# Performance work log

Measured on AMD Instinct MI355X. Metric: run time of the kernel, lower is better.

Reference implementation:

```python
import jax, jax.numpy as jnp
import numpy as np

N, E = 100000, 1600000          # nodes, edges
H, DH = 8, 256                  # heads, dim_hidden
D = DH // H                     # dim per head
NEG_SLOPE = 0.2                 # GAT leaky_relu slope
BETA = 0.5


def setup_inputs() -> dict:
    key = jax.random.key(0)
    ks = jax.random.split(key, 10)
    s = 1.0 / np.sqrt(DH)
    return {
        "x": jax.random.normal(ks[0], (N, DH), jnp.float32),
        "edge_index": jax.random.randint(ks[1], (2, E), 0, N, jnp.int32),
        "edge_attr": jax.random.uniform(ks[2], (E,), jnp.float32),
        # GAT params (no bias, add_self_loops=False)
        "Wg": jax.random.normal(ks[3], (DH, DH), jnp.float32) * s,
        "att_src": jax.random.normal(ks[4], (H, D), jnp.float32) * s,
        "att_dst": jax.random.normal(ks[5], (H, D), jnp.float32) * s,
        # h_lin
        "Wh": jax.random.normal(ks[6], (DH, DH), jnp.float32) * s,
        "bh": jnp.zeros((DH,), jnp.float32),
        # lin
        "Wl": jax.random.normal(ks[7], (DH, DH), jnp.float32) * s,
        "bl": jnp.zeros((DH,), jnp.float32),
        # LayerNorm
        "ln_g": jnp.ones((DH,), jnp.float32),
        "ln_b": jnp.zeros((DH,), jnp.float32),
        # beta gate (beta>=0 -> constant vector)
        "b_param": jnp.full((DH,), BETA, jnp.float32),
    }


def _layer_norm(v, g, b, eps=1e-5):
    mu = jnp.mean(v, axis=-1, keepdims=True)
    var = jnp.var(v, axis=-1, keepdims=True)
    return (v - mu) * jax.lax.rsqrt(var + eps) * g + b


def _weighted_gat(x, edge_index, edge_attr, Wg, att_src, att_dst):
    # GATConv with per-edge weights folded into the softmax numerator.
    xs = (x @ Wg).reshape(N, H, D)                       # [N,H,D]
    a_src = jnp.einsum("nhd,hd->nh", xs, att_src)        # [N,H]
    a_dst = jnp.einsum("nhd,hd->nh", xs, att_dst)
    src, dst = edge_index[0], edge_index[1]
    e = jax.nn.leaky_relu(a_src[src] + a_dst[dst], NEG_SLOPE)   # [E,H]
    m = jax.ops.segment_max(e, dst, num_segments=N)             # [N,H]
    m = jnp.where(jnp.isfinite(m), m, 0.0)                      # isolated nodes
    p = jnp.exp(e - m[dst]) * edge_attr[:, None]                # weighted exp
    denom = jax.ops.segment_sum(p, dst, num_segments=N)         # [N,H]
    alpha = p / (denom[dst] + 1e-16)                            # [E,H]
    msg = alpha[:, :, None] * xs[src]                           # [E,H,D]
    out = jax.ops.segment_sum(msg, dst, num_segments=N)         # [N,H,D]
    return out.reshape(N, DH)


def reference(x, edge_index, edge_attr, Wg, att_src, att_dst, Wh, bh, Wl, bl, ln_g, ln_b, b_param):
    x_in = x
    h = jax.nn.relu(x @ Wh + bh)
    xg = _weighted_gat(x, edge_index, edge_attr, Wg, att_src, att_dst) + (x @ Wl + bl)
    xg = jax.nn.relu(xg)                                  # dropout p=0 (eval)
    beta = b_param[None, :]
    out = (1.0 - beta) * _layer_norm(h * xg, ln_g, ln_b) + beta * xg
    return out + x_in                                     # residual=True
```

## Files before the change

### kernel.cpp

```cpp
#include <hip/hip_runtime.h>

typedef __attribute__((ext_vector_type(4))) float f32x4;
typedef __attribute__((ext_vector_type(8))) __bf16 bf16x8;

__device__ __forceinline__ unsigned short f2bf(float f) {
    return __builtin_bit_cast(unsigned short, (__bf16)f);
}
__device__ __forceinline__ float bf2f(unsigned short u) {
    return __builtin_bit_cast(float, (unsigned)u << 16);
}

__device__ __forceinline__ void gload16(const void* g, void* l) {
    __builtin_amdgcn_global_load_lds(
        (const __attribute__((address_space(1))) void*)g,
        (__attribute__((address_space(3))) void*)l, 16, 0, 0);
}

__global__ __launch_bounds__(256) void k_prep(
    const float* __restrict__ x, unsigned short* __restrict__ xb, long total, long totalPad,
    const float* __restrict__ Wg, const float* __restrict__ Wh, const float* __restrict__ Wl,
    unsigned short* __restrict__ wt,
    const int* __restrict__ dst, int E, int* __restrict__ deg,
    int nCvt, int nHist) {
    const int b = blockIdx.x;
    const int tid = threadIdx.x;
    if (b < nCvt) {
        long i = ((long)b * 256 + tid) * 4;
        if (i >= totalPad) return;
        if (i < total) {
            float4 v = *(const float4*)(x + i);
            ushort4 u;
            u.x = f2bf(v.x); u.y = f2bf(v.y); u.z = f2bf(v.z); u.w = f2bf(v.w);
            *(ushort4*)(xb + i) = u;
        } else {
            ushort4 u = {0, 0, 0, 0};
            *(ushort4*)(xb + i) = u;
        }
    } else if (b < nCvt + 768) {
        int t = (b - nCvt) * 256 + tid;
        int nn = t >> 8, k = t & 255;
        const float* W = (nn < 256) ? Wg : (nn < 512) ? Wh : Wl;
        wt[t] = f2bf(W[k * 256 + (nn & 255)]);
    } else {
        int bb = b - nCvt - 768;
        for (int e = bb * 256 + tid; e < E; e += nHist * 256)
            atomicAdd(&deg[dst[e]], 1);
    }
}

__global__ __launch_bounds__(256) void k_gemm(
    const unsigned short* __restrict__ A,
    const unsigned short* __restrict__ BT,
    unsigned short* __restrict__ xs, unsigned short* __restrict__ hb,
    unsigned short* __restrict__ xlb,
    const float* __restrict__ bh, const float* __restrict__ bl, int M, int nwg) {
    __shared__ unsigned short Al[128 * 32];
    __shared__ unsigned short Bl[128 * 32];
    const int bid = blockIdx.x;
    const int xcd = bid & 7, idx = bid >> 3;
    const int q = nwg >> 3, r = nwg & 7;
    const int wg = (xcd < r ? xcd * (q + 1) : r * (q + 1) + (xcd - r) * q) + idx;
    const int tm = wg / 6, tn = wg % 6;

    const int tid = threadIdx.x;
    const int lane = tid & 63;
    const int wave = tid >> 6;
    const int wm = (wave >> 1) * 64, wn = (wave & 1) * 64;

    f32x4 acc[4][4] = {};

    const int ml = tid & 15;
    const int kh = (tid >> 4) & 3;
    const int m0 = (tid >> 6) * 16 + ml;
    const unsigned short* Ag = A + (size_t)tm * 128 * 256 + (size_t)m0 * 256 + kh * 8;
    const unsigned short* Bg = BT + (size_t)tn * 128 * 256 + (size_t)m0 * 256 + kh * 8;

    const char* Ab = (const char*)Al + (wm >> 4) * 1024 + lane * 16;
    const char* Bb = (const char*)Bl + (wn >> 4) * 1024 + lane * 16;

    for (int ks = 0; ks < 8; ++ks) {
        const int k0 = ks * 32;
#pragma unroll
        for (int s = 0; s < 2; ++s) {
            gload16(Ag + (size_t)s * 64 * 256 + k0, (char*)Al + s * 4096 + wave * 1024 + (lane * 16));
            gload16(Bg + (size_t)s * 64 * 256 + k0, (char*)Bl + s * 4096 + wave * 1024 + (lane * 16));
        }
        __syncthreads();
        bf16x8 af[4], bfr[4];
#pragma unroll
        for (int i = 0; i < 4; ++i) {
            af[i]  = *(const bf16x8*)(Ab + i * 1024);
            bfr[i] = *(const bf16x8*)(Bb + i * 1024);
        }
#pragma unroll
        for (int i = 0; i < 4; ++i)
#pragma unroll
            for (int j = 0; j < 4; ++j)
                acc[i][j] = __builtin_amdgcn_mfma_f32_16x16x32_bf16(af[i], bfr[j], acc[i][j], 0, 0, 0);
        __syncthreads();
    }

    const int colbase = tn * 128 + wn;
    const int rbase = tm * 128 + wm + (lane >> 4) * 4;
#pragma unroll
    for (int i = 0; i < 4; ++i) {
#pragma unroll
        for (int j = 0; j < 4; ++j) {
            const int cg = colbase + j * 16 + (lane & 15);
#pragma unroll
            for (int q2 = 0; q2 < 4; ++q2) {
                const int rg = rbase + i * 16 + q2;
                if (rg < M) {
                    float v = acc[i][j][q2];
                    if (cg < 256) {
                        xs[(size_t)rg * 256 + cg] = f2bf(v);
                    } else if (cg < 512) {
                        float t = v + bh[cg - 256];
                        hb[(size_t)rg * 256 + (cg - 256)] = f2bf(t > 0.f ? t : 0.f);
                    } else {
                        xlb[(size_t)rg * 256 + (cg - 512)] = f2bf(v + bl[cg - 512]);
                    }
                }
            }
        }
    }
}

__global__ __launch_bounds__(256) void k_attn(const unsigned short* __restrict__ xs,
                                              const float* __restrict__ att_src,
                                              const float* __restrict__ att_dst,
                                              float* __restrict__ a_src,
                                              float* __restrict__ a_dst, int N) {
    int t = blockIdx.x * 256 + threadIdx.x;
    int n = t >> 3, hh = t & 7;
    if (n >= N) return;
    const ushort4* xp = (const ushort4*)(xs + (size_t)n * 256 + hh * 32);
    const float4* sp = (const float4*)(att_src + hh * 32);
    const float4* dp = (const float4*)(att_dst + hh * 32);
    float sa = 0.f, sd = 0.f;
#pragma unroll
    for (int q = 0; q < 8; ++q) {
        ushort4 u = xp[q];
        float4 s = sp[q], d = dp[q];
        float v0 = bf2f(u.x), v1 = bf2f(u.y), v2 = bf2f(u.z), v3 = bf2f(u.w);
        sa += v0 * s.x + v1 * s.y + v2 * s.z + v3 * s.w;
        sd += v0 * d.x + v1 * d.y + v2 * d.z + v3 * d.w;
    }
    a_src[t] = sa;
    a_dst[t] = sd;
}

__global__ __launch_bounds__(256) void k_scan1(const int* __restrict__ deg, int* __restrict__ offs,
                                               int* __restrict__ bsum, int Npad) {
    __shared__ int s[256];
    int t = threadIdx.x;
    int i = blockIdx.x * 256 + t;
    int v = (i < Npad) ? ((deg[i] + 7) & ~7) : 0;
    s[t] = v;
    __syncthreads();
#pragma unroll
    for (int off = 1; off < 256; off <<= 1) {
        int x = (t >= off) ? s[t - off] : 0;
        __syncthreads();
        s[t] += x;
        __syncthreads();
    }
    offs[i] = s[t] - v;
    if (t == 255) bsum[blockIdx.x] = s[255];
}

__global__ __launch_bounds__(512) void k_scan2(int* __restrict__ bsum, int nb) {
    __shared__ int s[512];
    int t = threadIdx.x;
    int v = (t < nb) ? bsum[t] : 0;
    s[t] = v;
    __syncthreads();
#pragma unroll
    for (int off = 1; off < 512; off <<= 1) {
        int x = (t >= off) ? s[t - off] : 0;
        __syncthreads();
        s[t] += x;
        __syncthreads();
    }
    if (t < nb) bsum[t] = s[t] - v;
}

__global__ __launch_bounds__(256) void k_scan3(int* __restrict__ offs, const int* __restrict__ bsum,
                                               int* __restrict__ cursor) {
    int i = blockIdx.x * 256 + threadIdx.x;
    int o = offs[i] + bsum[blockIdx.x];
    offs[i] = o;
    cursor[i] = o;
}

__global__ void k_edge(const int* __restrict__ ei, const float* __restrict__ ea, int E,
                       const float* __restrict__ a_src, const float* __restrict__ a_dst,
                       int* __restrict__ cursor, int* __restrict__ srcArr,
                       unsigned short* __restrict__ pvArr) {
    for (int e = blockIdx.x * blockDim.x + threadIdx.x; e < E; e += gridDim.x * blockDim.x) {
        const int s = ei[e];
        const int d = ei[(size_t)E + e];
        const float w = ea[e];
        const int pos = atomicAdd(&cursor[d], 1);
        const float4* As = (const float4*)(a_src + (size_t)s * 8);
        const float4* Ad = (const float4*)(a_dst + (size_t)d * 8);
        float4 s0 = As[0], s1 = As[1], d0 = Ad[0], d1 = Ad[1];
        float a[8] = {s0.x + d0.x, s0.y + d0.y, s0.z + d0.z, s0.w + d0.w,
                      s1.x + d1.x, s1.y + d1.y, s1.z + d1.z, s1.w + d1.w};
        unsigned pk[4];
#pragma unroll
        for (int h = 0; h < 4; ++h) {
            float lo = a[2 * h], hi = a[2 * h + 1];
            lo = (lo > 0.f) ? lo : 0.2f * lo;
            hi = (hi > 0.f) ? hi : 0.2f * hi;
            unsigned short plo = f2bf(__expf(lo) * w);
            unsigned short phi = f2bf(__expf(hi) * w);
            pk[h] = (unsigned)plo | ((unsigned)phi << 16);
        }
        srcArr[pos] = s;
        uint4 v = {pk[0], pk[1], pk[2], pk[3]};
        *(uint4*)(pvArr + (size_t)pos * 8) = v;
    }
}

__global__ __launch_bounds__(256) void k_agg(
    const int* __restrict__ offs, const int* __restrict__ deg,
    const int* __restrict__ srcArr, const unsigned short* __restrict__ pvArr,
    const unsigned short* __restrict__ xs, const unsigned short* __restrict__ hb,
    const unsigned short* __restrict__ xlb,
    const unsigned short* __restrict__ xbf, const float* __restrict__ ln_g,
    const float* __restrict__ ln_b,
    const float* __restrict__ beta, float* __restrict__ out, int N) {
    const int wave = threadIdx.x >> 6, lane = threadIdx.x & 63;
    const int n = blockIdx.x * 4 + wave;
    if (n >= N) return;
    const int start = offs[n];
    const int dpad = (deg[n] + 7) & ~7;
    const int head = lane >> 3;
    const int eSub = lane & 7;

    f32x4 acc = {0.f, 0.f, 0.f, 0.f};
    float dsum = 0.f;

    const int* sp = srcArr + start;
    const unsigned short* pp = pvArr + (size_t)start * 8 + head;
    const char* xsb = (const char*)xs;
    const unsigned rowoff = (unsigned)lane * 8;

    for (int g = 0; g < dpad; g += 8) {
        const int sA = sp[g + eSub];
        ushort4 rows[8];
        float pvv[8];
#pragma unroll
        for (int e = 0; e < 8; ++e)
            rows[e] = *(const ushort4*)(xsb + (size_t)(unsigned)__shfl(sA, e) * 512 + rowoff);
#pragma unroll
        for (int e = 0; e < 8; ++e)
            pvv[e] = bf2f(pp[(size_t)(g + e) * 8]);
#pragma unroll
        for (int e = 0; e < 8; ++e) {
            const float p = pvv[e];
            dsum += p;
            acc[0] += p * bf2f(rows[e].x);
            acc[1] += p * bf2f(rows[e].y);
            acc[2] += p * bf2f(rows[e].z);
            acc[3] += p * bf2f(rows[e].w);
        }
    }
    const float inv = 1.f / (dsum + 1e-16f);

    const size_t base = (size_t)n * 256 + lane * 4;
    ushort4 xlu = *(const ushort4*)(xlb + base);
    ushort4 hu = *(const ushort4*)(hb + base);
    ushort4 xiu = *(const ushort4*)(xbf + base);
    f32x4 xg, t4;
    float s1 = 0.f, s2 = 0.f;
    const float xl0[4] = {bf2f(xlu.x), bf2f(xlu.y), bf2f(xlu.z), bf2f(xlu.w)};
    const float hv0[4] = {bf2f(hu.x), bf2f(hu.y), bf2f(hu.z), bf2f(hu.w)};
    const float xi0[4] = {bf2f(xiu.x), bf2f(xiu.y), bf2f(xiu.z), bf2f(xiu.w)};
#pragma unroll
    for (int q = 0; q < 4; ++q) {
        float gg = acc[q] * inv + xl0[q];
        gg = gg > 0.f ? gg : 0.f;
        xg[q] = gg;
        float t = hv0[q] * gg;
        t4[q] = t;
        s1 += t;
        s2 += t * t;
    }
#pragma unroll
    for (int off = 32; off; off >>= 1) {
        s1 += __shfl_xor(s1, off);
        s2 += __shfl_xor(s2, off);
    }
    const float mu = s1 * (1.f / 256.f);
    const float var = s2 * (1.f / 256.f) - mu * mu;
    const float rs = rsqrtf(var + 1e-5f);

    f32x4 g4 = *(const f32x4*)(ln_g + lane * 4);
    f32x4 b4 = *(const f32x4*)(ln_b + lane * 4);
    f32x4 be = *(const f32x4*)(beta + lane * 4);
    f32x4 o;
#pragma unroll
    for (int q = 0; q < 4; ++q) {
        float ln = (t4[q] - mu) * rs * g4[q] + b4[q];
        o[q] = (1.f - be[q]) * ln + be[q] * xg[q] + xi0[q];
    }
    *(f32x4*)(out + base) = o;
}

extern "C" void kernel_launch(void* const* d_in, const int* in_sizes, int n_in,
                              void* d_out, int out_size, void* d_ws, size_t ws_size,
                              hipStream_t stream) {
    const float* x = (const float*)d_in[0];
    const int* ei = (const int*)d_in[1];
    const float* ea = (const float*)d_in[2];
    const float* Wg = (const float*)d_in[3];
    const float* att_src = (const float*)d_in[4];
    const float* att_dst = (const float*)d_in[5];
    const float* Wh = (const float*)d_in[6];
    const float* bh = (const float*)d_in[7];
    const float* Wl = (const float*)d_in[8];
    const float* bl = (const float*)d_in[9];
    const float* ln_g = (const float*)d_in[10];
    const float* ln_b = (const float*)d_in[11];
    const float* beta = (const float*)d_in[12];
    float* out = (float*)d_out;

    const int DH = 256;
    const int N = in_sizes[0] / DH;
    const int E = in_sizes[2];
    const int Mpad = ((N + 127) / 128) * 128;
    const int Npad = ((N + 255) / 256) * 256;
    const int nscanb = Npad / 256;
    const int nwg = (Mpad / 128) * 6;
    const int nCvt = Mpad / 4;
    const int nHist = 2048;
    const size_t Epad = (size_t)E + 8 * (size_t)N;

    char* w = (char*)d_ws;
    auto take = [&](size_t bytes) -> char* {
        char* p = w;
        w += (bytes + 255) & ~(size_t)255;
        return p;
    };
    unsigned short* xs = (unsigned short*)take((size_t)N * DH * 2);
    unsigned short* hb = (unsigned short*)take((size_t)N * DH * 2);
    unsigned short* xlb = (unsigned short*)take((size_t)N * DH * 2);
    float* a_src = (float*)take((size_t)N * 8 * 4);
    float* a_dst = (float*)take((size_t)N * 8 * 4);
    unsigned short* xbf = (unsigned short*)take((size_t)Mpad * DH * 2);
    unsigned short* wt = (unsigned short*)take((size_t)768 * 256 * 2);
    int* deg = (int*)take((size_t)Npad * 4);
    int* offs = (int*)take((size_t)Npad * 4);
    int* cursor = (int*)take((size_t)Npad * 4);
    int* bsum = (int*)take(512 * 4);
    int* srcArr = (int*)take(Epad * 4);
    unsigned short* pvArr = (unsigned short*)take(Epad * 8 * 2);

    hipMemsetAsync(deg, 0, (size_t)Npad * 4, stream);
    hipMemsetAsync(srcArr, 0, Epad * 4, stream);
    hipMemsetAsync(pvArr, 0, Epad * 8 * 2, stream);

    k_prep<<<nCvt + 768 + nHist, 256, 0, stream>>>(x, xbf, (long)N * DH, (long)Mpad * DH,
                                                   Wg, Wh, Wl, wt, ei + E, E, deg, nCvt, nHist);

    k_scan1<<<nscanb, 256, 0, stream>>>(deg, offs, bsum, Npad);
    k_scan2<<<1, 512, 0, stream>>>(bsum, nscanb);
    k_scan3<<<nscanb, 256, 0, stream>>>(offs, bsum, cursor);

    k_gemm<<<nwg, 256, 0, stream>>>(xbf, wt, xs, hb, xlb, bh, bl, N, nwg);

    k_attn<<<(N * 8 + 255) / 256, 256, 0, stream>>>(xs, att_src, att_dst, a_src, a_dst, N);

    k_edge<<<2048, 256, 0, stream>>>(ei, ea, E, a_src, a_dst, cursor, srcArr, pvArr);

    k_agg<<<(N + 3) / 4, 256, 0, stream>>>(offs, deg, srcArr, pvArr,
                                           xs, hb, xlb, xbf, ln_g, ln_b, beta, out, N);
}
```

Measured before the change: 606.8 us.

## Restructure GEMM to 8 waves, double-buffer A in LDS, read B from global

The GEMM block grows to 512 threads, with each wave computing a 32x64 sub-tile. The A tile is double-buffered in LDS so the next k-slice loads while the current one computes, dropping one barrier per iteration. B fragments now come straight from global memory, relying on cache, instead of being staged through LDS. The epilogue picks the output buffer and bias once per block rather than branching per element. The risks are extra global and L2 traffic for B and higher register pressure from direct global loads.

```diff
diff --git a/kernel.cpp b/kernel.cpp
--- a/kernel.cpp
+++ b/kernel.cpp
@@ -48,14 +48,13 @@
     }
 }
 
-__global__ __launch_bounds__(256) void k_gemm(
+__global__ __launch_bounds__(512) void k_gemm(
     const unsigned short* __restrict__ A,
     const unsigned short* __restrict__ BT,
     unsigned short* __restrict__ xs, unsigned short* __restrict__ hb,
     unsigned short* __restrict__ xlb,
     const float* __restrict__ bh, const float* __restrict__ bl, int M, int nwg) {
-    __shared__ unsigned short Al[128 * 32];
-    __shared__ unsigned short Bl[128 * 32];
+    __shared__ unsigned short Al[2][4096];
     const int bid = blockIdx.x;
     const int xcd = bid & 7, idx = bid >> 3;
     const int q = nwg >> 3, r = nwg & 7;
@@ -65,61 +64,67 @@
     const int tid = threadIdx.x;
     const int lane = tid & 63;
     const int wave = tid >> 6;
-    const int wm = (wave >> 1) * 64, wn = (wave & 1) * 64;
-
-    f32x4 acc[4][4] = {};
-
-    const int ml = tid & 15;
+    const int wm = (wave >> 1) * 32;
+    const int wn = (wave & 1) * 64;
+    const int colbase = tn * 128 + wn;
+    const int fr = lane & 15;
+    const int ko = (lane >> 4) * 8;
+
+    f32x4 acc[2][4] = {};
+
+    const int m0 = (tid >> 6) * 16 + (tid & 15);
     const int kh = (tid >> 4) & 3;
-    const int m0 = (tid >> 6) * 16 + ml;
     const unsigned short* Ag = A + (size_t)tm * 128 * 256 + (size_t)m0 * 256 + kh * 8;
-    const unsigned short* Bg = BT + (size_t)tn * 128 * 256 + (size_t)m0 * 256 + kh * 8;
-
-    const char* Ab = (const char*)Al + (wm >> 4) * 1024 + lane * 16;
-    const char* Bb = (const char*)Bl + (wn >> 4) * 1024 + lane * 16;
+    char* dst0 = (char*)Al[0] + tid * 16;
+    char* dst1 = (char*)Al[1] + tid * 16;
+
+    const char* ab0 = (const char*)Al[0] + (wm >> 4) * 1024 + lane * 16;
+    const char* ab1 = (const char*)Al[1] + (wm >> 4) * 1024 + lane * 16;
+    const unsigned short* Bg = BT + (size_t)(colbase + fr) * 256 + ko;
+
+    gload16(Ag, dst0);
+    __syncthreads();
 
     for (int ks = 0; ks < 8; ++ks) {
-        const int k0 = ks * 32;
-#pragma unroll
-        for (int s = 0; s < 2; ++s) {
-            gload16(Ag + (size_t)s * 64 * 256 + k0, (char*)Al + s * 4096 + wave * 1024 + (lane * 16));
-            gload16(Bg + (size_t)s * 64 * 256 + k0, (char*)Bl + s * 4096 + wave * 1024 + (lane * 16));
-        }
-        __syncthreads();
-        bf16x8 af[4], bfr[4];
-#pragma unroll
-        for (int i = 0; i < 4; ++i) {
-            af[i]  = *(const bf16x8*)(Ab + i * 1024);
-            bfr[i] = *(const bf16x8*)(Bb + i * 1024);
-        }
-#pragma unroll
-        for (int i = 0; i < 4; ++i)
+        const int cur = ks & 1;
+        if (ks < 7)
+            gload16(Ag + (ks + 1) * 32, cur ? dst0 : dst1);
+
+        bf16x8 bfr[4], af[2];
+#pragma unroll
+        for (int j = 0; j < 4; ++j)
+            bfr[j] = *(const bf16x8*)(Bg + (size_t)j * 16 * 256 + ks * 32);
+        const char* ab = cur ? ab1 : ab0;
+#pragma unroll
+        for (int i = 0; i < 2; ++i)
+            af[i] = *(const bf16x8*)(ab + i * 1024);
+
+#pragma unroll
+        for (int i = 0; i < 2; ++i)
 #pragma unroll
             for (int j = 0; j < 4; ++j)
                 acc[i][j] = __builtin_amdgcn_mfma_f32_16x16x32_bf16(af[i], bfr[j], acc[i][j], 0, 0, 0);
-        __syncthreads();
-    }
-
-    const int colbase = tn * 128 + wn;
+
+        __syncthreads();
+    }
+
+    const int ob = tn >> 1;
+    unsigned short* obuf = (ob == 0) ? xs : (ob == 1) ? hb : xlb;
+    const float* bias = (ob == 1) ? bh : bl;
     const int rbase = tm * 128 + wm + (lane >> 4) * 4;
 #pragma unroll
-    for (int i = 0; i < 4; ++i) {
+    for (int i = 0; i < 2; ++i) {
 #pragma unroll
         for (int j = 0; j < 4; ++j) {
-            const int cg = colbase + j * 16 + (lane & 15);
+            const int c0 = (tn & 1) * 128 + wn + j * 16 + fr;
+            float bv = (ob == 0) ? 0.f : bias[c0];
 #pragma unroll
             for (int q2 = 0; q2 < 4; ++q2) {
                 const int rg = rbase + i * 16 + q2;
                 if (rg < M) {
-                    float v = acc[i][j][q2];
-                    if (cg < 256) {
-                        xs[(size_t)rg * 256 + cg] = f2bf(v);
-                    } else if (cg < 512) {
-                        float t = v + bh[cg - 256];
-                        hb[(size_t)rg * 256 + (cg - 256)] = f2bf(t > 0.f ? t : 0.f);
-                    } else {
-                        xlb[(size_t)rg * 256 + (cg - 512)] = f2bf(v + bl[cg - 512]);
-                    }
+                    float v = acc[i][j][q2] + bv;
+                    if (ob == 1) v = v > 0.f ? v : 0.f;
+                    obuf[(size_t)rg * 256 + c0] = f2bf(v);
                 }
             }
         }
@@ -369,7 +374,7 @@
     k_scan2<<<1, 512, 0, stream>>>(bsum, nscanb);
     k_scan3<<<nscanb, 256, 0, stream>>>(offs, bsum, cursor);
 
-    k_gemm<<<nwg, 256, 0, stream>>>(xbf, wt, xs, hb, xlb, bh, bl, N, nwg);
+    k_gemm<<<nwg, 512, 0, stream>>>(xbf, wt, xs, hb, xlb, bh, bl, N, nwg);
 
     k_attn<<<(N * 8 + 255) / 256, 256, 0, stream>>>(xs, att_src, att_dst, a_src, a_dst, N);
 
```

New measurement: 630.7 us. 1.04x slower.
